# Kernel optimization log

Hardware: AMD Instinct MI355X
Metric: run time of the kernel (lower is better)

## Reference

```python
import jax, jax.numpy as jnp
import numpy as np

DECAY = 0.99
EPS = 1e-05
TEMP = 1.0


def setup_inputs() -> dict:
    key = jax.random.key(0)
    k1, k2, k3 = jax.random.split(key, 3)
    B, T, D, C = 64, 512, 256, 1024
    x = jax.random.normal(k1, (B, T, D), dtype=jnp.float32)
    embed = jax.random.normal(k2, (1, C, D), dtype=jnp.float32)
    embed_avg = jax.random.normal(k3, (1, C, D), dtype=jnp.float32)
    cluster_size = jnp.ones((1, C), dtype=jnp.float32)
    return {"x": x, "embed": embed, "embed_avg": embed_avg, "cluster_size": cluster_size}


def reference(x, embed, embed_avg, cluster_size):
    B, T, D = x.shape
    H, C, _ = embed.shape  # H = num_codebooks = 1
    flatten = x.reshape(H, B * T, D)  # pack_one 'h * d'
    e = jax.lax.stop_gradient(embed)  # learnable_codebook = False

    dist = (2.0 * jnp.einsum('hnd,hcd->hnc', flatten, e)
            - jnp.sum(flatten * flatten, axis=-1, keepdims=True)
            - jnp.sum(e * e, axis=-1)[:, None, :])  # [h, N, C]

    # gumbel_sample: deterministic argmax + straight-through one-hot
    embed_ind = jnp.argmax(dist, axis=-1)  # [h, N]
    probs = jax.nn.softmax(dist / TEMP, axis=-1)
    hard = jax.nn.one_hot(embed_ind, C, dtype=dist.dtype)
    embed_onehot = probs + jax.lax.stop_gradient(hard - probs)  # [h, N, C]

    # quantize via onehot matmul (training path)
    quantize = jnp.einsum('hnc,hcd->hnd', embed_onehot, e).reshape(B, T, D)

    # EMA codebook update
    cs_new = DECAY * cluster_size + (1.0 - DECAY) * embed_onehot.sum(axis=1)  # [h, C]
    embed_sum = jnp.einsum('hnd,hnc->hcd', flatten, embed_onehot)  # [h, C, D]
    ea_new = DECAY * embed_avg + (1.0 - DECAY) * embed_sum
    n = jnp.sum(cs_new, axis=-1, keepdims=True)
    cs_smoothed = (cs_new + EPS) / (n + C * EPS) * n  # laplace smoothing * n
    embed_norm = ea_new / cs_smoothed[..., None]  # new codebook [h, C, D]

    return (quantize, embed_ind.reshape(B, T), embed_norm, cs_new)
```

## Files before the change

kernel.cpp:

```cpp
#include <hip/hip_runtime.h>
#include <cstdint>

#define DECAY 0.99f
#define OMD   0.01f
#define EPSV  1e-5f

constexpr int N_PTS   = 32768;
constexpr int D_DIM   = 256;
constexpr int C_CODES = 1024;
constexpr int KPACK   = 768;

constexpr int PG = 4;
constexpr int PK = 8;
constexpr int LCAP = 8192;

typedef _Float16 half8  __attribute__((ext_vector_type(8)));
typedef _Float16 half4v __attribute__((ext_vector_type(4)));
typedef float    floatx4 __attribute__((ext_vector_type(4)));

constexpr size_t WS_ENORM = 0;
constexpr size_t WS_CSSUM = 1024;
constexpr size_t WS_PCNT  = 2048;
constexpr size_t WS_CAND  = 8192;
constexpr size_t WS_A16   = WS_CAND + 1048576;
constexpr size_t WS_B16   = WS_A16 + 12582912;
constexpr size_t WS_TOTAL_FLOATS = WS_B16 + 393216;

__device__ __forceinline__ void async_copy16(const void* g, void* s) {
    __builtin_amdgcn_global_load_lds(
        (const __attribute__((address_space(1))) unsigned int*)(uintptr_t)g,
        (__attribute__((address_space(3))) unsigned int*)(uintptr_t)s, 16, 0, 0);
}

__global__ __launch_bounds__(256) void vq_prep_x(const float* __restrict__ X,
                                                 _Float16* __restrict__ A) {
    int i = blockIdx.x * 256 + threadIdx.x;
    int n = i >> 6, kq = (i & 63) * 4;
    float4 v = reinterpret_cast<const float4*>(X)[i];
    _Float16 h0 = (_Float16)v.x, h1 = (_Float16)v.y, h2 = (_Float16)v.z, h3 = (_Float16)v.w;
    _Float16 l0 = (_Float16)(v.x - (float)h0), l1 = (_Float16)(v.y - (float)h1);
    _Float16 l2 = (_Float16)(v.z - (float)h2), l3 = (_Float16)(v.w - (float)h3);
    half4v hi = {h0, h1, h2, h3};
    half4v lo = {l0, l1, l2, l3};
    _Float16* row = A + (size_t)n * KPACK;
    *reinterpret_cast<half4v*>(row + kq)       = hi;
    *reinterpret_cast<half4v*>(row + 256 + kq) = hi;
    *reinterpret_cast<half4v*>(row + 512 + kq) = lo;
}

__global__ __launch_bounds__(256) void vq_prep_e(const float* __restrict__ E,
                                                 _Float16* __restrict__ B) {
    int i = blockIdx.x * 256 + threadIdx.x;
    int c = i >> 6, kq = (i & 63) * 4;
    float4 v = reinterpret_cast<const float4*>(E)[i];
    _Float16 h0 = (_Float16)v.x, h1 = (_Float16)v.y, h2 = (_Float16)v.z, h3 = (_Float16)v.w;
    _Float16 l0 = (_Float16)(v.x - (float)h0), l1 = (_Float16)(v.y - (float)h1);
    _Float16 l2 = (_Float16)(v.z - (float)h2), l3 = (_Float16)(v.w - (float)h3);
    half4v hi = {h0, h1, h2, h3};
    half4v lo = {l0, l1, l2, l3};
    _Float16* row = B + (size_t)c * KPACK;
    *reinterpret_cast<half4v*>(row + kq)       = hi;
    *reinterpret_cast<half4v*>(row + 256 + kq) = lo;
    *reinterpret_cast<half4v*>(row + 512 + kq) = hi;
}

__global__ __launch_bounds__(256) void vq_enorm(const float* __restrict__ E,
                                                float* __restrict__ enorm) {
    int c    = blockIdx.x * 4 + (threadIdx.x >> 6);
    int lane = threadIdx.x & 63;
    float4 v = reinterpret_cast<const float4*>(E)[c * 64 + lane];
    float s  = v.x * v.x + v.y * v.y + v.z * v.z + v.w * v.w;
#pragma unroll
    for (int off = 32; off > 0; off >>= 1) s += __shfl_down(s, off, 64);
    if (lane == 0) enorm[c] = s;
}

__global__ __launch_bounds__(1024) void vq_cssum(const float* __restrict__ cs_in,
                                                 float* __restrict__ out) {
    __shared__ float red[1024];
    int t = threadIdx.x;
    red[t] = cs_in[t];
    __syncthreads();
    for (int s = 512; s > 0; s >>= 1) {
        if (t < s) red[t] += red[t + s];
        __syncthreads();
    }
    if (t == 0) out[0] = red[0];
}

__global__ __launch_bounds__(256, 2) void vq_gemm(
    const _Float16* __restrict__ A, const _Float16* __restrict__ B,
    const float* __restrict__ enorm, float2* __restrict__ cand) {
    __shared__ _Float16 As[128 * 64];
    __shared__ _Float16 Bs[128 * 64];

    const int L      = blockIdx.x;
    const int within = L >> 3;
    const int ct     = within & 7;
    const int rt     = (L & 7) | ((within >> 3) << 3);
    const int n0     = rt * 128;
    const int cb0    = ct * 128;

    const int tid = threadIdx.x;
    const int w   = tid >> 6;
    const int l   = tid & 63;

    const int srow = l >> 3;
    const int sq   = (l & 7) ^ srow;

    floatx4 acc[4][4] = {};

    for (int k0 = 0; k0 < KPACK; k0 += 64) {
        __syncthreads();
#pragma unroll
        for (int t = 0; t < 4; ++t) {
            int rr = w * 32 + t * 8;
            const _Float16* ga = A + (size_t)(n0 + rr + srow) * KPACK + k0 + sq * 8;
            async_copy16(ga, &As[rr * 64]);
            const _Float16* gb = B + (size_t)(cb0 + rr + srow) * KPACK + k0 + sq * 8;
            async_copy16(gb, &Bs[rr * 64]);
        }
        __syncthreads();
#pragma unroll
        for (int kk = 0; kk < 2; ++kk) {
            half8 af[4], bf[4];
            int qa = kk * 4 + (l >> 4);
#pragma unroll
            for (int i = 0; i < 4; ++i) {
                int row  = (w & 1) * 64 + 16 * i + (l & 15);
                af[i] = *reinterpret_cast<const half8*>(&As[row * 64 + (qa ^ (row & 7)) * 8]);
                int crow = (w >> 1) * 64 + 16 * i + (l & 15);
                bf[i] = *reinterpret_cast<const half8*>(&Bs[crow * 64 + (qa ^ (crow & 7)) * 8]);
            }
#pragma unroll
            for (int i = 0; i < 4; ++i)
#pragma unroll
                for (int j = 0; j < 4; ++j)
                    acc[i][j] = __builtin_amdgcn_mfma_f32_16x16x32_f16(af[i], bf[j], acc[i][j], 0, 0, 0);
        }
    }

    const int colbase = cb0 + (w >> 1) * 64 + (l & 15);
    float en[4];
#pragma unroll
    for (int j = 0; j < 4; ++j) en[j] = enorm[colbase + 16 * j];

#pragma unroll
    for (int i = 0; i < 4; ++i) {
#pragma unroll
        for (int reg = 0; reg < 4; ++reg) {
            float bv = -3.4e38f;
            int   bi = 0x7fffffff;
#pragma unroll
            for (int j = 0; j < 4; ++j) {
                float v = 2.0f * acc[i][j][reg] - en[j];
                int   c = colbase + 16 * j;
                if (v > bv || (v == bv && c < bi)) { bv = v; bi = c; }
            }
#pragma unroll
            for (int s = 1; s < 16; s <<= 1) {
                float ov = __shfl_xor(bv, s, 64);
                int   oi = __shfl_xor(bi, s, 64);
                if (ov > bv || (ov == bv && oi < bi)) { bv = ov; bi = oi; }
            }
            if ((l & 15) == 0) {
                int row = n0 + (w & 1) * 64 + 16 * i + (l >> 4) * 4 + reg;
                cand[(size_t)row * 16 + ct * 2 + (w >> 1)] = make_float2(bv, (float)bi);
            }
        }
    }
}

__global__ __launch_bounds__(256) void vq_merge3(
    const float2* __restrict__ cand, const float* __restrict__ E,
    float* __restrict__ quant, float* __restrict__ indout) {
    __shared__ int rowsel[64];
    const int tid = threadIdx.x;
    const int n0  = blockIdx.x * 64;

    if (tid < 64) {
        int r = n0 + tid;
        float bv = -3.4e38f;
        int   bi = 0x7fffffff;
#pragma unroll
        for (int t = 0; t < 16; ++t) {
            float2 cv = cand[(size_t)r * 16 + t];
            int ci = (int)cv.y;
            if (cv.x > bv || (cv.x == bv && ci < bi)) { bv = cv.x; bi = ci; }
        }
        bi &= (C_CODES - 1);
        rowsel[tid] = bi;
        indout[r]   = (float)bi;
    }
    __syncthreads();

    const float4* E4 = reinterpret_cast<const float4*>(E);
    float4*       Q4 = reinterpret_cast<float4*>(quant);
    const int lane = tid & 63;
#pragma unroll
    for (int it = 0; it < 16; ++it) {
        int r   = (tid >> 6) + 4 * it;
        int idx = rowsel[r];
        Q4[(n0 + r) * 64 + lane] = E4[idx * 64 + lane];
    }
}

__global__ __launch_bounds__(256) void vq_part(
    const float* __restrict__ X, const float* __restrict__ indf,
    float* __restrict__ P, int* __restrict__ pcnt) {
    __shared__ int list[LCAP];
    __shared__ int cnt[PK];
    __shared__ int lcnt;
    const int cg = blockIdx.x;
    const int g  = blockIdx.y;
    const int t  = threadIdx.x;
    if (t == 0) lcnt = 0;
    if (t < PK) cnt[t] = 0;
    __syncthreads();

    const float4* I4 = reinterpret_cast<const float4*>(indf);
    float4 v[8];
#pragma unroll
    for (int j = 0; j < 8; ++j)
        v[j] = I4[g * 2048 + j * 256 + t];

#pragma unroll
    for (int j = 0; j < 8; ++j) {
        int base = (g * 2048 + j * 256 + t) * 4;
        int k0 = (int)v[j].x, k1 = (int)v[j].y, k2 = (int)v[j].z, k3 = (int)v[j].w;
        if ((k0 >> 3) == cg) { int p = atomicAdd(&lcnt, 1); atomicAdd(&cnt[k0 & 7], 1); if (p < LCAP) list[p] = ((base + 0) << 3) | (k0 & 7); }
        if ((k1 >> 3) == cg) { int p = atomicAdd(&lcnt, 1); atomicAdd(&cnt[k1 & 7], 1); if (p < LCAP) list[p] = ((base + 1) << 3) | (k1 & 7); }
        if ((k2 >> 3) == cg) { int p = atomicAdd(&lcnt, 1); atomicAdd(&cnt[k2 & 7], 1); if (p < LCAP) list[p] = ((base + 2) << 3) | (k2 & 7); }
        if ((k3 >> 3) == cg) { int p = atomicAdd(&lcnt, 1); atomicAdd(&cnt[k3 & 7], 1); if (p < LCAP) list[p] = ((base + 3) << 3) | (k3 & 7); }
    }
    __syncthreads();

    int m = lcnt; if (m > LCAP) m = LCAP;
    float acc[PK] = {0, 0, 0, 0, 0, 0, 0, 0};
    int r = 0;
    for (; r + 8 <= m; r += 8) {
        int e[8];
        float val[8];
#pragma unroll
        for (int q = 0; q < 8; ++q) e[q] = list[r + q];
#pragma unroll
        for (int q = 0; q < 8; ++q) val[q] = X[(size_t)(e[q] >> 3) * D_DIM + t];
#pragma unroll
        for (int q = 0; q < 8; ++q) {
            int k = e[q] & 7;
#pragma unroll
            for (int kk = 0; kk < PK; ++kk) acc[kk] += (k == kk) ? val[q] : 0.0f;
        }
    }
    for (; r < m; ++r) {
        int e = list[r];
        float val = X[(size_t)(e >> 3) * D_DIM + t];
        int k = e & 7;
#pragma unroll
        for (int kk = 0; kk < PK; ++kk) acc[kk] += (k == kk) ? val : 0.0f;
    }

#pragma unroll
    for (int kk = 0; kk < PK; ++kk)
        P[((size_t)g * C_CODES + cg * PK + kk) * D_DIM + t] = acc[kk];
    if (t < PK) pcnt[g * C_CODES + cg * PK + t] = cnt[t];
}

__global__ __launch_bounds__(256) void vq_comb(
    const float* __restrict__ P, const int* __restrict__ pcnt,
    const float* __restrict__ ea, const float* __restrict__ cs_in,
    const float* __restrict__ cs_sum,
    float* __restrict__ emb_norm, float* __restrict__ cs_out) {
    const int c = blockIdx.x;
    const int t = threadIdx.x;
    float s = 0.0f;
#pragma unroll
    for (int g = 0; g < PG; ++g)
        s += P[((size_t)g * C_CODES + c) * D_DIM + t];
    int total = pcnt[c] + pcnt[C_CODES + c] + pcnt[2 * C_CODES + c] + pcnt[3 * C_CODES + c];
    float cs    = DECAY * cs_in[c] + OMD * (float)total;
    float ntot  = DECAY * cs_sum[0] + OMD * (float)N_PTS;
    float denom = (cs + EPSV) / (ntot + (float)C_CODES * EPSV) * ntot;
    emb_norm[(size_t)c * D_DIM + t] =
        (DECAY * ea[(size_t)c * D_DIM + t] + OMD * s) / denom;
    if (t == 0) cs_out[c] = cs;
}

__global__ __launch_bounds__(256) void vq_main_fb(
    const float* __restrict__ X, const float* __restrict__ E,
    const float* __restrict__ enorm,
    float* __restrict__ quant, float* __restrict__ indout,
    float* __restrict__ counts, float* __restrict__ esum) {
    constexpr int BN = 64, BC = 64, BK = 32, PADR = 68;
    __shared__ float As[BK * PADR];
    __shared__ float Bs[BK * PADR];
    __shared__ float redv[BN * 16];
    __shared__ int   redi[BN * 16];
    __shared__ int   rowsel[BN];

    const int tid = threadIdx.x;
    const int n0  = blockIdx.x * BN;
    const int tr  = tid >> 4;
    const int tc  = tid & 15;
    const int sr  = tid >> 2;
    const int sk  = tid & 3;

    const float4* X4 = reinterpret_cast<const float4*>(X);
    const float4* E4 = reinterpret_cast<const float4*>(E);

    float best[4];
    int   bidx[4];
#pragma unroll
    for (int i = 0; i < 4; i++) { best[i] = -3.4e38f; bidx[i] = 0; }

    for (int c0 = 0; c0 < C_CODES; c0 += BC) {
        float acc[4][4] = {};
        for (int k0 = 0; k0 < D_DIM; k0 += BK) {
            __syncthreads();
#pragma unroll
            for (int it = 0; it < 2; ++it) {
                int   k4 = sk + 4 * it;
                float4 av = X4[(n0 + sr) * 64 + (k0 >> 2) + k4];
                float4 bv = E4[(c0 + sr) * 64 + (k0 >> 2) + k4];
                int kk = k4 * 4;
                As[(kk + 0) * PADR + sr] = av.x;
                As[(kk + 1) * PADR + sr] = av.y;
                As[(kk + 2) * PADR + sr] = av.z;
                As[(kk + 3) * PADR + sr] = av.w;
                Bs[(kk + 0) * PADR + sr] = bv.x;
                Bs[(kk + 1) * PADR + sr] = bv.y;
                Bs[(kk + 2) * PADR + sr] = bv.z;
                Bs[(kk + 3) * PADR + sr] = bv.w;
            }
            __syncthreads();
#pragma unroll
            for (int k = 0; k < BK; ++k) {
                float4 a = *reinterpret_cast<const float4*>(&As[k * PADR + 4 * tr]);
                float4 b = *reinterpret_cast<const float4*>(&Bs[k * PADR + 4 * tc]);
                acc[0][0] += a.x * b.x; acc[0][1] += a.x * b.y;
                acc[0][2] += a.x * b.z; acc[0][3] += a.x * b.w;
                acc[1][0] += a.y * b.x; acc[1][1] += a.y * b.y;
                acc[1][2] += a.y * b.z; acc[1][3] += a.y * b.w;
                acc[2][0] += a.z * b.x; acc[2][1] += a.z * b.y;
                acc[2][2] += a.z * b.z; acc[2][3] += a.z * b.w;
                acc[3][0] += a.w * b.x; acc[3][1] += a.w * b.y;
                acc[3][2] += a.w * b.z; acc[3][3] += a.w * b.w;
            }
        }
        float4 en = *reinterpret_cast<const float4*>(&enorm[c0 + 4 * tc]);
        float enj[4] = {en.x, en.y, en.z, en.w};
#pragma unroll
        for (int i = 0; i < 4; i++)
#pragma unroll
            for (int j = 0; j < 4; j++) {
                float v = 2.0f * acc[i][j] - enj[j];
                int   c = c0 + 4 * tc + j;
                if (v > best[i]) { best[i] = v; bidx[i] = c; }
            }
    }

    __syncthreads();
#pragma unroll
    for (int i = 0; i < 4; i++) {
        redv[(4 * tr + i) * 16 + tc] = best[i];
        redi[(4 * tr + i) * 16 + tc] = bidx[i];
    }
    __syncthreads();
    if (tid < BN) {
        float bv = redv[tid * 16];
        int   bi = redi[tid * 16];
        for (int t = 1; t < 16; t++) {
            float v  = redv[tid * 16 + t];
            int   id = redi[tid * 16 + t];
            if (v > bv || (v == bv && id < bi)) { bv = v; bi = id; }
        }
        rowsel[tid] = bi;
        indout[n0 + tid] = (float)bi;
        unsafeAtomicAdd(&counts[bi], 1.0f);
    }
    __syncthreads();

    float4*   Q4   = reinterpret_cast<float4*>(quant);
    const int lane = tid & 63;
#pragma unroll
    for (int it = 0; it < 16; ++it) {
        int r   = (tid >> 6) + 4 * it;
        int idx = rowsel[r];
        float4 ev = E4[idx * 64 + lane];
        Q4[(n0 + r) * 64 + lane] = ev;
        float4 xv = X4[(n0 + r) * 64 + lane];
        float* dst = &esum[idx * D_DIM + lane * 4];
        unsafeAtomicAdd(dst + 0, xv.x);
        unsafeAtomicAdd(dst + 1, xv.y);
        unsafeAtomicAdd(dst + 2, xv.z);
        unsafeAtomicAdd(dst + 3, xv.w);
    }
}

__global__ __launch_bounds__(1024) void vq_fin1(const float* __restrict__ cs_in,
                                                const float* __restrict__ counts,
                                                float* __restrict__ cs_out,
                                                float* __restrict__ denom) {
    __shared__ float red[1024];
    int   c  = threadIdx.x;
    float cs = DECAY * cs_in[c] + OMD * counts[c];
    cs_out[c] = cs;
    red[c]    = cs;
    __syncthreads();
    for (int s = 512; s > 0; s >>= 1) {
        if (c < s) red[c] += red[c + s];
        __syncthreads();
    }
    float ntot = red[0];
    denom[c] = (cs + EPSV) / (ntot + (float)C_CODES * EPSV) * ntot;
}

__global__ __launch_bounds__(256) void vq_fin2(const float* __restrict__ ea,
                                               const float* __restrict__ esum,
                                               const float* __restrict__ denom,
                                               float* __restrict__ out) {
    int i = blockIdx.x * 256 + threadIdx.x;
    int c = i >> 6;
    float4 a = reinterpret_cast<const float4*>(ea)[i];
    float4 s = reinterpret_cast<const float4*>(esum)[i];
    float  d = denom[c];
    float4 o;
    o.x = (DECAY * a.x + OMD * s.x) / d;
    o.y = (DECAY * a.y + OMD * s.y) / d;
    o.z = (DECAY * a.z + OMD * s.z) / d;
    o.w = (DECAY * a.w + OMD * s.w) / d;
    reinterpret_cast<float4*>(out)[i] = o;
}

extern "C" void kernel_launch(void* const* d_in, const int* in_sizes, int n_in,
                              void* d_out, int out_size, void* d_ws, size_t ws_size,
                              hipStream_t stream) {
    const float* x            = (const float*)d_in[0];
    const float* embed        = (const float*)d_in[1];
    const float* embed_avg    = (const float*)d_in[2];
    const float* cluster_size = (const float*)d_in[3];

    float* out      = (float*)d_out;
    float* quant    = out;
    float* ind      = out + (size_t)N_PTS * D_DIM;
    float* emb_norm = ind + N_PTS;
    float* cs_out   = emb_norm + (size_t)C_CODES * D_DIM;

    float* ws    = (float*)d_ws;
    float* enorm = ws + WS_ENORM;

    vq_enorm<<<C_CODES / 4, 256, 0, stream>>>(embed, enorm);

    if (ws_size >= WS_TOTAL_FLOATS * sizeof(float)) {
        float*    cssum = ws + WS_CSSUM;
        int*      pcnt  = (int*)(ws + WS_PCNT);
        float2*   cand  = (float2*)(ws + WS_CAND);
        float*    P     = ws + WS_CAND;
        _Float16* A16   = (_Float16*)(ws + WS_A16);
        _Float16* B16   = (_Float16*)(ws + WS_B16);

        vq_cssum<<<1, 1024, 0, stream>>>(cluster_size, cssum);
        vq_prep_x<<<N_PTS * 64 / 256, 256, 0, stream>>>(x, A16);
        vq_prep_e<<<C_CODES * 64 / 256, 256, 0, stream>>>(embed, B16);
        vq_gemm<<<2048, 256, 0, stream>>>(A16, B16, enorm, cand);
        vq_merge3<<<N_PTS / 64, 256, 0, stream>>>(cand, embed, quant, ind);
        vq_part<<<dim3(C_CODES / PK, PG), 256, 0, stream>>>(x, ind, P, pcnt);
        vq_comb<<<C_CODES, 256, 0, stream>>>(P, pcnt, embed_avg, cluster_size, cssum,
                                             emb_norm, cs_out);
    } else {
        float* countsf = ws + WS_CAND;
        float* esum    = ws + WS_CAND + 1024;
        float* denom   = ws + WS_A16;
        hipMemsetAsync(countsf, 0, (1024 + (size_t)C_CODES * D_DIM) * sizeof(float), stream);
        vq_main_fb<<<N_PTS / 64, 256, 0, stream>>>(x, embed, enorm, quant, ind, countsf, esum);
        vq_fin1<<<1, 1024, 0, stream>>>(cluster_size, countsf, cs_out, denom);
        vq_fin2<<<(C_CODES * D_DIM / 4) / 256, 256, 0, stream>>>(embed_avg, esum, denom, emb_norm);
    }
}
```

Baseline: 223.2 us.

## Enlarge GEMM tile to 256x256 with double-buffered async pipeline, fuse small kernels

Rewrites the distance GEMM to use 512-thread blocks computing 256x256 tiles with double-buffered LDS, async global-to-LDS staging interleaved with MFMA phases, and setprio hints. This raises data reuse per tile and overlaps loads with compute. It also folds the codebook norm computation into prep_e and the cluster_size sum into vq_comb, removing two launches. The larger tile uses more LDS and registers, which lowers occupancy, and vq_comb now redoes the cluster_size reduction in every block.

```diff
diff --git a/kernel.cpp b/kernel.cpp
--- a/kernel.cpp
+++ b/kernel.cpp
@@ -9,6 +9,7 @@
 constexpr int D_DIM   = 256;
 constexpr int C_CODES = 1024;
 constexpr int KPACK   = 768;
+constexpr int NKT     = 12;
 
 constexpr int PG = 4;
 constexpr int PK = 8;
@@ -49,7 +50,8 @@
 }
 
 __global__ __launch_bounds__(256) void vq_prep_e(const float* __restrict__ E,
-                                                 _Float16* __restrict__ B) {
+                                                 _Float16* __restrict__ B,
+                                                 float* __restrict__ enorm) {
     int i = blockIdx.x * 256 + threadIdx.x;
     int c = i >> 6, kq = (i & 63) * 4;
     float4 v = reinterpret_cast<const float4*>(E)[i];
@@ -62,6 +64,11 @@
     *reinterpret_cast<half4v*>(row + kq)       = hi;
     *reinterpret_cast<half4v*>(row + 256 + kq) = lo;
     *reinterpret_cast<half4v*>(row + 512 + kq) = hi;
+    float s = v.x * v.x + v.y * v.y + v.z * v.z + v.w * v.w;
+    int lane = threadIdx.x & 63;
+#pragma unroll
+    for (int off = 32; off > 0; off >>= 1) s += __shfl_down(s, off, 64);
+    if (lane == 0) enorm[c] = s;
 }
 
 __global__ __launch_bounds__(256) void vq_enorm(const float* __restrict__ E,
@@ -75,78 +82,121 @@
     if (lane == 0) enorm[c] = s;
 }
 
-__global__ __launch_bounds__(1024) void vq_cssum(const float* __restrict__ cs_in,
-                                                 float* __restrict__ out) {
-    __shared__ float red[1024];
-    int t = threadIdx.x;
-    red[t] = cs_in[t];
-    __syncthreads();
-    for (int s = 512; s > 0; s >>= 1) {
-        if (t < s) red[t] += red[t + s];
-        __syncthreads();
-    }
-    if (t == 0) out[0] = red[0];
-}
-
-__global__ __launch_bounds__(256, 2) void vq_gemm(
+__device__ __forceinline__ void stage_half(const _Float16* __restrict__ G,
+                                           int grow0, int k0,
+                                           _Float16* lds_base, int tid) {
+    const int w  = tid >> 6, l = tid & 63;
+    const int rr = w * 8 + (l >> 3);
+    const int cq = (l & 7) ^ (l >> 3);
+#pragma unroll
+    for (int L = 0; L < 2; ++L) {
+        const _Float16* src = G + (size_t)(grow0 + L * 64 + rr) * KPACK + k0 + cq * 8;
+        async_copy16(src, lds_base + (size_t)(L * 64 + w * 8) * 64);
+    }
+}
+
+__global__ __launch_bounds__(512, 2) void vq_gemm(
     const _Float16* __restrict__ A, const _Float16* __restrict__ B,
     const float* __restrict__ enorm, float2* __restrict__ cand) {
-    __shared__ _Float16 As[128 * 64];
-    __shared__ _Float16 Bs[128 * 64];
-
-    const int L      = blockIdx.x;
-    const int within = L >> 3;
-    const int ct     = within & 7;
-    const int rt     = (L & 7) | ((within >> 3) << 3);
-    const int n0     = rt * 128;
-    const int cb0    = ct * 128;
+    __shared__ _Float16 As[2][256][64];
+    __shared__ _Float16 Bs[2][256][64];
+
+    const int L  = blockIdx.x;
+    const int ct = (L >> 3) & 3;
+    const int rt = (L & 7) | ((L >> 5) << 3);
+    const int n0  = rt * 256;
+    const int cb0 = ct * 256;
 
     const int tid = threadIdx.x;
-    const int w   = tid >> 6;
-    const int l   = tid & 63;
-
-    const int srow = l >> 3;
-    const int sq   = (l & 7) ^ srow;
-
-    floatx4 acc[4][4] = {};
-
-    for (int k0 = 0; k0 < KPACK; k0 += 64) {
-        __syncthreads();
-#pragma unroll
-        for (int t = 0; t < 4; ++t) {
-            int rr = w * 32 + t * 8;
-            const _Float16* ga = A + (size_t)(n0 + rr + srow) * KPACK + k0 + sq * 8;
-            async_copy16(ga, &As[rr * 64]);
-            const _Float16* gb = B + (size_t)(cb0 + rr + srow) * KPACK + k0 + sq * 8;
-            async_copy16(gb, &Bs[rr * 64]);
+    const int w  = tid >> 6, l = tid & 63;
+    const int wr = w >> 2;
+    const int wc = w & 3;
+
+    floatx4 acc[8][4] = {};
+    half8   bf[4][2];
+
+    stage_half(A, n0,        0,  &As[0][0][0],   tid);
+    stage_half(A, n0 + 128,  0,  &As[0][128][0], tid);
+    stage_half(B, cb0,       0,  &Bs[0][0][0],   tid);
+    stage_half(B, cb0 + 128, 0,  &Bs[0][128][0], tid);
+    stage_half(B, cb0,       64, &Bs[1][0][0],   tid);
+    stage_half(B, cb0 + 128, 64, &Bs[1][128][0], tid);
+    asm volatile("s_waitcnt vmcnt(4)" ::: "memory");
+    __builtin_amdgcn_s_barrier();
+    __builtin_amdgcn_sched_barrier(0);
+
+#pragma unroll 1
+    for (int it = 0; it < 6; ++it) {
+        const int t0 = 2 * it;
+        const int kA1 = (t0 + 1) * 64;
+        const int kT2 = ((t0 + 2 < NKT) ? (t0 + 2) : (NKT - 1)) * 64;
+        const int kT3 = ((t0 + 3 < NKT) ? (t0 + 3) : (NKT - 1)) * 64;
+#pragma unroll
+        for (int hb = 0; hb < 2; ++hb) {
+#pragma unroll
+            for (int g = 0; g < 4; ++g) {
+                if (g == 0) {
+#pragma unroll
+                    for (int j = 0; j < 4; ++j)
+#pragma unroll
+                        for (int ks = 0; ks < 2; ++ks) {
+                            const int col = wc * 64 + 16 * j + (l & 15);
+                            const int qa  = ks * 4 + (l >> 4);
+                            bf[j][ks] = *reinterpret_cast<const half8*>(
+                                &Bs[hb][col][(qa ^ (col & 7)) * 8]);
+                        }
+                }
+                half8 af[2][2];
+#pragma unroll
+                for (int ii = 0; ii < 2; ++ii)
+#pragma unroll
+                    for (int ks = 0; ks < 2; ++ks) {
+                        const int row = wr * 128 + 32 * g + 16 * ii + (l & 15);
+                        const int qa  = ks * 4 + (l >> 4);
+                        af[ii][ks] = *reinterpret_cast<const half8*>(
+                            &As[hb][row][(qa ^ (row & 7)) * 8]);
+                    }
+                const int ph = hb * 4 + g;
+                if (ph == 0)      stage_half(A, n0,        kA1, &As[1][0][0],   tid);
+                else if (ph == 1) stage_half(A, n0 + 128,  kA1, &As[1][128][0], tid);
+                else if (ph == 2) stage_half(B, cb0,       kT2, &Bs[0][0][0],   tid);
+                else if (ph == 3) stage_half(B, cb0 + 128, kT2, &Bs[0][128][0], tid);
+                else if (ph == 4) stage_half(A, n0,        kT2, &As[0][0][0],   tid);
+                else if (ph == 5) stage_half(A, n0 + 128,  kT2, &As[0][128][0], tid);
+                else if (ph == 6) stage_half(B, cb0,       kT3, &Bs[1][0][0],   tid);
+                else              stage_half(B, cb0 + 128, kT3, &Bs[1][128][0], tid);
+
+                __builtin_amdgcn_s_barrier();
+                __builtin_amdgcn_sched_barrier(0);
+
+                __builtin_amdgcn_s_setprio(1);
+#pragma unroll
+                for (int ii = 0; ii < 2; ++ii)
+#pragma unroll
+                    for (int j = 0; j < 4; ++j)
+#pragma unroll
+                        for (int ks = 0; ks < 2; ++ks)
+                            acc[2 * g + ii][j] = __builtin_amdgcn_mfma_f32_16x16x32_f16(
+                                af[ii][ks], bf[j][ks], acc[2 * g + ii][j], 0, 0, 0);
+                __builtin_amdgcn_s_setprio(0);
+
+                if (ph == 3 || ph == 7)
+                    asm volatile("s_waitcnt vmcnt(4)" ::: "memory");
+                __builtin_amdgcn_s_barrier();
+                __builtin_amdgcn_sched_barrier(0);
+            }
         }
-        __syncthreads();
-#pragma unroll
-        for (int kk = 0; kk < 2; ++kk) {
-            half8 af[4], bf[4];
-            int qa = kk * 4 + (l >> 4);
-#pragma unroll
-            for (int i = 0; i < 4; ++i) {
-                int row  = (w & 1) * 64 + 16 * i + (l & 15);
-                af[i] = *reinterpret_cast<const half8*>(&As[row * 64 + (qa ^ (row & 7)) * 8]);
-                int crow = (w >> 1) * 64 + 16 * i + (l & 15);
-                bf[i] = *reinterpret_cast<const half8*>(&Bs[crow * 64 + (qa ^ (crow & 7)) * 8]);
-            }
-#pragma unroll
-            for (int i = 0; i < 4; ++i)
-#pragma unroll
-                for (int j = 0; j < 4; ++j)
-                    acc[i][j] = __builtin_amdgcn_mfma_f32_16x16x32_f16(af[i], bf[j], acc[i][j], 0, 0, 0);
-        }
-    }
-
-    const int colbase = cb0 + (w >> 1) * 64 + (l & 15);
+    }
+
+    asm volatile("s_waitcnt vmcnt(0)" ::: "memory");
+
+    const int colbase = cb0 + wc * 64 + (l & 15);
     float en[4];
 #pragma unroll
     for (int j = 0; j < 4; ++j) en[j] = enorm[colbase + 16 * j];
 
 #pragma unroll
-    for (int i = 0; i < 4; ++i) {
+    for (int i = 0; i < 8; ++i) {
 #pragma unroll
         for (int reg = 0; reg < 4; ++reg) {
             float bv = -3.4e38f;
@@ -164,8 +214,8 @@
                 if (ov > bv || (ov == bv && oi < bi)) { bv = ov; bi = oi; }
             }
             if ((l & 15) == 0) {
-                int row = n0 + (w & 1) * 64 + 16 * i + (l >> 4) * 4 + reg;
-                cand[(size_t)row * 16 + ct * 2 + (w >> 1)] = make_float2(bv, (float)bi);
+                int row = n0 + wr * 128 + 16 * i + (l >> 4) * 4 + reg;
+                cand[(size_t)row * 16 + ct * 4 + wc] = make_float2(bv, (float)bi);
             }
         }
     }
@@ -269,17 +319,25 @@
 __global__ __launch_bounds__(256) void vq_comb(
     const float* __restrict__ P, const int* __restrict__ pcnt,
     const float* __restrict__ ea, const float* __restrict__ cs_in,
-    const float* __restrict__ cs_sum,
     float* __restrict__ emb_norm, float* __restrict__ cs_out) {
+    __shared__ float red[256];
     const int c = blockIdx.x;
     const int t = threadIdx.x;
+    red[t] = cs_in[t] + cs_in[t + 256] + cs_in[t + 512] + cs_in[t + 768];
+    __syncthreads();
+    for (int st = 128; st > 0; st >>= 1) {
+        if (t < st) red[t] += red[t + st];
+        __syncthreads();
+    }
+    const float cssum = red[0];
+
     float s = 0.0f;
 #pragma unroll
     for (int g = 0; g < PG; ++g)
         s += P[((size_t)g * C_CODES + c) * D_DIM + t];
     int total = pcnt[c] + pcnt[C_CODES + c] + pcnt[2 * C_CODES + c] + pcnt[3 * C_CODES + c];
     float cs    = DECAY * cs_in[c] + OMD * (float)total;
-    float ntot  = DECAY * cs_sum[0] + OMD * (float)N_PTS;
+    float ntot  = DECAY * cssum + OMD * (float)N_PTS;
     float denom = (cs + EPSV) / (ntot + (float)C_CODES * EPSV) * ntot;
     emb_norm[(size_t)c * D_DIM + t] =
         (DECAY * ea[(size_t)c * D_DIM + t] + OMD * s) / denom;
@@ -449,25 +507,22 @@
     float* ws    = (float*)d_ws;
     float* enorm = ws + WS_ENORM;
 
-    vq_enorm<<<C_CODES / 4, 256, 0, stream>>>(embed, enorm);
-
     if (ws_size >= WS_TOTAL_FLOATS * sizeof(float)) {
-        float*    cssum = ws + WS_CSSUM;
         int*      pcnt  = (int*)(ws + WS_PCNT);
         float2*   cand  = (float2*)(ws + WS_CAND);
         float*    P     = ws + WS_CAND;
         _Float16* A16   = (_Float16*)(ws + WS_A16);
         _Float16* B16   = (_Float16*)(ws + WS_B16);
 
-        vq_cssum<<<1, 1024, 0, stream>>>(cluster_size, cssum);
         vq_prep_x<<<N_PTS * 64 / 256, 256, 0, stream>>>(x, A16);
-        vq_prep_e<<<C_CODES * 64 / 256, 256, 0, stream>>>(embed, B16);
-        vq_gemm<<<2048, 256, 0, stream>>>(A16, B16, enorm, cand);
+        vq_prep_e<<<C_CODES * 64 / 256, 256, 0, stream>>>(embed, B16, enorm);
+        vq_gemm<<<512, 512, 0, stream>>>(A16, B16, enorm, cand);
         vq_merge3<<<N_PTS / 64, 256, 0, stream>>>(cand, embed, quant, ind);
         vq_part<<<dim3(C_CODES / PK, PG), 256, 0, stream>>>(x, ind, P, pcnt);
-        vq_comb<<<C_CODES, 256, 0, stream>>>(P, pcnt, embed_avg, cluster_size, cssum,
+        vq_comb<<<C_CODES, 256, 0, stream>>>(P, pcnt, embed_avg, cluster_size,
                                              emb_norm, cs_out);
     } else {
+        vq_enorm<<<C_CODES / 4, 256, 0, stream>>>(embed, enorm);
         float* countsf = ws + WS_CAND;
         float* esum    = ws + WS_CAND + 1024;
         float* denom   = ws + WS_A16;
```

Measured after the change: 227.6 us. No clear change (+2.0%).

## Store hi/lo split once and remap K-tiles; fuse prep, enorm and cssum kernels

Applied to the files above, without the earlier changes.

The fp16 hi/lo split buffers now hold only [hi, lo] per row instead of a three-segment packed copy. The GEMM K loop maps its 12 tiles onto these 512-wide rows with index arithmetic, which cuts prep write traffic and workspace size by a third. The x/embed prep and codebook-norm kernels are merged into one launch, the cluster-size sum is folded into the combine kernel (each block redoes a small reduction), and GEMM launch bounds now ask for 3 blocks per CU. The higher occupancy target may force register spills.

```diff
diff --git a/kernel.cpp b/kernel.cpp
--- a/kernel.cpp
+++ b/kernel.cpp
@@ -8,7 +8,9 @@
 constexpr int N_PTS   = 32768;
 constexpr int D_DIM   = 256;
 constexpr int C_CODES = 1024;
-constexpr int KPACK   = 768;
+constexpr int NKT     = 12;
+constexpr int AP      = 512;
+constexpr int BP      = 512;
 
 constexpr int PG = 4;
 constexpr int PK = 8;
@@ -19,12 +21,11 @@
 typedef float    floatx4 __attribute__((ext_vector_type(4)));
 
 constexpr size_t WS_ENORM = 0;
-constexpr size_t WS_CSSUM = 1024;
 constexpr size_t WS_PCNT  = 2048;
 constexpr size_t WS_CAND  = 8192;
 constexpr size_t WS_A16   = WS_CAND + 1048576;
-constexpr size_t WS_B16   = WS_A16 + 12582912;
-constexpr size_t WS_TOTAL_FLOATS = WS_B16 + 393216;
+constexpr size_t WS_B16   = WS_A16 + 8388608;
+constexpr size_t WS_TOTAL_FLOATS = WS_B16 + 262144;
 
 __device__ __forceinline__ void async_copy16(const void* g, void* s) {
     __builtin_amdgcn_global_load_lds(
@@ -32,36 +33,41 @@
         (__attribute__((address_space(3))) unsigned int*)(uintptr_t)s, 16, 0, 0);
 }
 
-__global__ __launch_bounds__(256) void vq_prep_x(const float* __restrict__ X,
-                                                 _Float16* __restrict__ A) {
-    int i = blockIdx.x * 256 + threadIdx.x;
-    int n = i >> 6, kq = (i & 63) * 4;
-    float4 v = reinterpret_cast<const float4*>(X)[i];
-    _Float16 h0 = (_Float16)v.x, h1 = (_Float16)v.y, h2 = (_Float16)v.z, h3 = (_Float16)v.w;
-    _Float16 l0 = (_Float16)(v.x - (float)h0), l1 = (_Float16)(v.y - (float)h1);
-    _Float16 l2 = (_Float16)(v.z - (float)h2), l3 = (_Float16)(v.w - (float)h3);
-    half4v hi = {h0, h1, h2, h3};
-    half4v lo = {l0, l1, l2, l3};
-    _Float16* row = A + (size_t)n * KPACK;
-    *reinterpret_cast<half4v*>(row + kq)       = hi;
-    *reinterpret_cast<half4v*>(row + 256 + kq) = hi;
-    *reinterpret_cast<half4v*>(row + 512 + kq) = lo;
-}
-
-__global__ __launch_bounds__(256) void vq_prep_e(const float* __restrict__ E,
-                                                 _Float16* __restrict__ B) {
-    int i = blockIdx.x * 256 + threadIdx.x;
-    int c = i >> 6, kq = (i & 63) * 4;
-    float4 v = reinterpret_cast<const float4*>(E)[i];
-    _Float16 h0 = (_Float16)v.x, h1 = (_Float16)v.y, h2 = (_Float16)v.z, h3 = (_Float16)v.w;
-    _Float16 l0 = (_Float16)(v.x - (float)h0), l1 = (_Float16)(v.y - (float)h1);
-    _Float16 l2 = (_Float16)(v.z - (float)h2), l3 = (_Float16)(v.w - (float)h3);
-    half4v hi = {h0, h1, h2, h3};
-    half4v lo = {l0, l1, l2, l3};
-    _Float16* row = B + (size_t)c * KPACK;
-    *reinterpret_cast<half4v*>(row + kq)       = hi;
-    *reinterpret_cast<half4v*>(row + 256 + kq) = lo;
-    *reinterpret_cast<half4v*>(row + 512 + kq) = hi;
+__global__ __launch_bounds__(256) void vq_prep(const float* __restrict__ X,
+                                               const float* __restrict__ E,
+                                               _Float16* __restrict__ A,
+                                               _Float16* __restrict__ B,
+                                               float* __restrict__ enorm) {
+    if (blockIdx.x < 8192) {
+        int i = blockIdx.x * 256 + threadIdx.x;
+        int n = i >> 6, kq = (i & 63) * 4;
+        float4 v = reinterpret_cast<const float4*>(X)[i];
+        _Float16 h0 = (_Float16)v.x, h1 = (_Float16)v.y, h2 = (_Float16)v.z, h3 = (_Float16)v.w;
+        _Float16 l0 = (_Float16)(v.x - (float)h0), l1 = (_Float16)(v.y - (float)h1);
+        _Float16 l2 = (_Float16)(v.z - (float)h2), l3 = (_Float16)(v.w - (float)h3);
+        half4v hi = {h0, h1, h2, h3};
+        half4v lo = {l0, l1, l2, l3};
+        _Float16* row = A + (size_t)n * AP;
+        *reinterpret_cast<half4v*>(row + kq)       = hi;
+        *reinterpret_cast<half4v*>(row + 256 + kq) = lo;
+    } else {
+        int i = (blockIdx.x - 8192) * 256 + threadIdx.x;
+        int c = i >> 6, kq = (i & 63) * 4;
+        float4 v = reinterpret_cast<const float4*>(E)[i];
+        _Float16 h0 = (_Float16)v.x, h1 = (_Float16)v.y, h2 = (_Float16)v.z, h3 = (_Float16)v.w;
+        _Float16 l0 = (_Float16)(v.x - (float)h0), l1 = (_Float16)(v.y - (float)h1);
+        _Float16 l2 = (_Float16)(v.z - (float)h2), l3 = (_Float16)(v.w - (float)h3);
+        half4v hi = {h0, h1, h2, h3};
+        half4v lo = {l0, l1, l2, l3};
+        _Float16* row = B + (size_t)c * BP;
+        *reinterpret_cast<half4v*>(row + kq)       = hi;
+        *reinterpret_cast<half4v*>(row + 256 + kq) = lo;
+        float s = v.x * v.x + v.y * v.y + v.z * v.z + v.w * v.w;
+        int lane = threadIdx.x & 63;
+#pragma unroll
+        for (int off = 32; off > 0; off >>= 1) s += __shfl_down(s, off, 64);
+        if (lane == 0) enorm[c] = s;
+    }
 }
 
 __global__ __launch_bounds__(256) void vq_enorm(const float* __restrict__ E,
@@ -75,20 +81,7 @@
     if (lane == 0) enorm[c] = s;
 }
 
-__global__ __launch_bounds__(1024) void vq_cssum(const float* __restrict__ cs_in,
-                                                 float* __restrict__ out) {
-    __shared__ float red[1024];
-    int t = threadIdx.x;
-    red[t] = cs_in[t];
-    __syncthreads();
-    for (int s = 512; s > 0; s >>= 1) {
-        if (t < s) red[t] += red[t + s];
-        __syncthreads();
-    }
-    if (t == 0) out[0] = red[0];
-}
-
-__global__ __launch_bounds__(256, 2) void vq_gemm(
+__global__ __launch_bounds__(256, 3) void vq_gemm(
     const _Float16* __restrict__ A, const _Float16* __restrict__ B,
     const float* __restrict__ enorm, float2* __restrict__ cand) {
     __shared__ _Float16 As[128 * 64];
@@ -110,14 +103,16 @@
 
     floatx4 acc[4][4] = {};
 
-    for (int k0 = 0; k0 < KPACK; k0 += 64) {
+    for (int kt = 0; kt < NKT; ++kt) {
+        const int ka = ((kt < 8) ? (kt & 3) : (kt - 4)) * 64;
+        const int kb = (kt < 4) ? kt * 64 : (kt < 8 ? 256 + (kt - 4) * 64 : (kt - 8) * 64);
         __syncthreads();
 #pragma unroll
         for (int t = 0; t < 4; ++t) {
             int rr = w * 32 + t * 8;
-            const _Float16* ga = A + (size_t)(n0 + rr + srow) * KPACK + k0 + sq * 8;
+            const _Float16* ga = A + (size_t)(n0 + rr + srow) * AP + ka + sq * 8;
             async_copy16(ga, &As[rr * 64]);
-            const _Float16* gb = B + (size_t)(cb0 + rr + srow) * KPACK + k0 + sq * 8;
+            const _Float16* gb = B + (size_t)(cb0 + rr + srow) * BP + kb + sq * 8;
             async_copy16(gb, &Bs[rr * 64]);
         }
         __syncthreads();
@@ -269,17 +264,25 @@
 __global__ __launch_bounds__(256) void vq_comb(
     const float* __restrict__ P, const int* __restrict__ pcnt,
     const float* __restrict__ ea, const float* __restrict__ cs_in,
-    const float* __restrict__ cs_sum,
     float* __restrict__ emb_norm, float* __restrict__ cs_out) {
+    __shared__ float red[256];
     const int c = blockIdx.x;
     const int t = threadIdx.x;
+    red[t] = cs_in[t] + cs_in[t + 256] + cs_in[t + 512] + cs_in[t + 768];
+    __syncthreads();
+    for (int st = 128; st > 0; st >>= 1) {
+        if (t < st) red[t] += red[t + st];
+        __syncthreads();
+    }
+    const float cssum = red[0];
+
     float s = 0.0f;
 #pragma unroll
     for (int g = 0; g < PG; ++g)
         s += P[((size_t)g * C_CODES + c) * D_DIM + t];
     int total = pcnt[c] + pcnt[C_CODES + c] + pcnt[2 * C_CODES + c] + pcnt[3 * C_CODES + c];
     float cs    = DECAY * cs_in[c] + OMD * (float)total;
-    float ntot  = DECAY * cs_sum[0] + OMD * (float)N_PTS;
+    float ntot  = DECAY * cssum + OMD * (float)N_PTS;
     float denom = (cs + EPSV) / (ntot + (float)C_CODES * EPSV) * ntot;
     emb_norm[(size_t)c * D_DIM + t] =
         (DECAY * ea[(size_t)c * D_DIM + t] + OMD * s) / denom;
@@ -449,25 +452,21 @@
     float* ws    = (float*)d_ws;
     float* enorm = ws + WS_ENORM;
 
-    vq_enorm<<<C_CODES / 4, 256, 0, stream>>>(embed, enorm);
-
     if (ws_size >= WS_TOTAL_FLOATS * sizeof(float)) {
-        float*    cssum = ws + WS_CSSUM;
         int*      pcnt  = (int*)(ws + WS_PCNT);
         float2*   cand  = (float2*)(ws + WS_CAND);
         float*    P     = ws + WS_CAND;
         _Float16* A16   = (_Float16*)(ws + WS_A16);
         _Float16* B16   = (_Float16*)(ws + WS_B16);
 
-        vq_cssum<<<1, 1024, 0, stream>>>(cluster_size, cssum);
-        vq_prep_x<<<N_PTS * 64 / 256, 256, 0, stream>>>(x, A16);
-        vq_prep_e<<<C_CODES * 64 / 256, 256, 0, stream>>>(embed, B16);
+        vq_prep<<<8448, 256, 0, stream>>>(x, embed, A16, B16, enorm);
         vq_gemm<<<2048, 256, 0, stream>>>(A16, B16, enorm, cand);
         vq_merge3<<<N_PTS / 64, 256, 0, stream>>>(cand, embed, quant, ind);
         vq_part<<<dim3(C_CODES / PK, PG), 256, 0, stream>>>(x, ind, P, pcnt);
-        vq_comb<<<C_CODES, 256, 0, stream>>>(P, pcnt, embed_avg, cluster_size, cssum,
+        vq_comb<<<C_CODES, 256, 0, stream>>>(P, pcnt, embed_avg, cluster_size,
                                              emb_norm, cs_out);
     } else {
+        vq_enorm<<<C_CODES / 4, 256, 0, stream>>>(embed, enorm);
         float* countsf = ws + WS_CAND;
         float* esum    = ws + WS_CAND + 1024;
         float* denom   = ws + WS_A16;
```

Measured after the change: 225.0 us. No clear change (+0.8%).
